# Kernel optimization log

Hardware: AMD Instinct MI355X
Metric: run time of the kernel (lower is better)

## Reference

```python
import jax, jax.numpy as jnp
import numpy as np

N_NODES = 100000
N_EDGES = 800000
IN_CH, HID_CH, OUT_CH = 128, 256, 128


def setup_inputs() -> dict:
    key = jax.random.key(0)
    ks = jax.random.split(key, 8)
    x = jax.random.normal(ks[0], (N_NODES, IN_CH), dtype=jnp.float32)
    edge_index = jax.random.randint(ks[1], (2, N_EDGES), 0, N_NODES, dtype=jnp.int64)
    def lin(k, fan_in, fan_out):
        bound = 1.0 / np.sqrt(fan_in)
        return jax.random.uniform(k, (fan_out, fan_in), minval=-bound, maxval=bound, dtype=jnp.float32)
    # PyG SAGEConv: lin_l (neighbor branch, with bias), lin_r (root branch, no bias)
    W1l = lin(ks[2], IN_CH, HID_CH)
    b1l = jnp.zeros((HID_CH,), dtype=jnp.float32)
    W1r = lin(ks[3], IN_CH, HID_CH)
    W2l = lin(ks[4], HID_CH, OUT_CH)
    b2l = jnp.zeros((OUT_CH,), dtype=jnp.float32)
    W2r = lin(ks[5], HID_CH, OUT_CH)
    return {"x": x, "edge_index": edge_index, "W1l": W1l, "b1l": b1l, "W1r": W1r,
            "W2l": W2l, "b2l": b2l, "W2r": W2r}


def _sage_conv(x, src, dst, Wl, bl, Wr):
    # mean-aggregate messages x[src] at dst, then lin_l(agg) + lin_r(x)
    msgs = x[src]                                        # [E, C]
    summed = jax.ops.segment_sum(msgs, dst, num_segments=N_NODES)
    cnt = jax.ops.segment_sum(jnp.ones((src.shape[0],), dtype=x.dtype), dst, num_segments=N_NODES)
    mean = summed / jnp.maximum(cnt, 1.0)[:, None]       # [N, C]
    return mean @ Wl.T + bl + x @ Wr.T


def reference(x, edge_index, W1l, b1l, W1r, W2l, b2l, W2r):
    src, dst = edge_index[0], edge_index[1]
    h = _sage_conv(x, src, dst, W1l, b1l, W1r)
    h = jax.nn.relu(h)
    # dropout is identity in eval mode (F.dropout with training=False)
    out = _sage_conv(h, src, dst, W2l, b2l, W2r)
    return out
```

## Files before the change

kernel.cpp:

```cpp
#include <hip/hip_runtime.h>

#define N_NODES 100000
#define N_EDGES 800000
#define SCAN_CHUNK 1024
#define SCAN_NB ((N_NODES + SCAN_CHUNK - 1) / SCAN_CHUNK)
#define ROWS_PER_BLK 391
#define TILES 25

typedef __attribute__((ext_vector_type(8))) _Float16 f16x8;
typedef __attribute__((ext_vector_type(4))) _Float16 f16x4;
typedef __attribute__((ext_vector_type(4))) float f32x4;

__global__ void count_int_k(const int* __restrict__ dst, int* __restrict__ cnt, int E) {
    int i = blockIdx.x * blockDim.x + threadIdx.x;
    if (i < E) atomicAdd(&cnt[dst[i]], 1);
}

__global__ __launch_bounds__(256) void scan1_k(const int* __restrict__ cnt,
                                               int* __restrict__ offs,
                                               int* __restrict__ bsums, int N) {
    __shared__ int s[256];
    int t = threadIdx.x;
    int base = blockIdx.x * SCAN_CHUNK + t * 4;
    int v0 = (base + 0 < N) ? cnt[base + 0] : 0;
    int v1 = (base + 1 < N) ? cnt[base + 1] : 0;
    int v2 = (base + 2 < N) ? cnt[base + 2] : 0;
    int v3 = (base + 3 < N) ? cnt[base + 3] : 0;
    int tsum = v0 + v1 + v2 + v3;
    s[t] = tsum;
    __syncthreads();
    for (int off = 1; off < 256; off <<= 1) {
        int val = (t >= off) ? s[t - off] : 0;
        __syncthreads();
        s[t] += val;
        __syncthreads();
    }
    int excl = s[t] - tsum;
    if (base + 0 < N) offs[base + 0] = excl;
    if (base + 1 < N) offs[base + 1] = excl + v0;
    if (base + 2 < N) offs[base + 2] = excl + v0 + v1;
    if (base + 3 < N) offs[base + 3] = excl + v0 + v1 + v2;
    if (t == 255) bsums[blockIdx.x] = s[255];
}

__global__ __launch_bounds__(256) void scan2_k(const int* __restrict__ bsums,
                                               int* __restrict__ boffs, int nb) {
    __shared__ int s[256];
    int t = threadIdx.x;
    int v = (t < nb) ? bsums[t] : 0;
    s[t] = v;
    __syncthreads();
    for (int off = 1; off < 256; off <<= 1) {
        int val = (t >= off) ? s[t - off] : 0;
        __syncthreads();
        s[t] += val;
        __syncthreads();
    }
    if (t < nb) boffs[t] = s[t] - v;
}

__global__ void scan3_k(int* __restrict__ offs, int* __restrict__ cursor,
                        const int* __restrict__ boffs, int N, int E) {
    int i = blockIdx.x * blockDim.x + threadIdx.x;
    if (i < N) {
        int v = offs[i] + boffs[i >> 10];
        offs[i] = v;
        cursor[i] = v;
    }
    if (i == 0) offs[N] = E;
}

__global__ void fill_k(const int* __restrict__ src, const int* __restrict__ dst,
                       int* __restrict__ cursor, int* __restrict__ perm, int E) {
    int e = blockIdx.x * blockDim.x + threadIdx.x;
    if (e < E) {
        int d = dst[e];
        int slot = atomicAdd(&cursor[d], 1);
        perm[slot] = src[e];
    }
}

__global__ __launch_bounds__(256) void cvt_f16_k(const float* __restrict__ in,
                                                 _Float16* __restrict__ outp, int n8) {
    int i = blockIdx.x * blockDim.x + threadIdx.x;
    if (i >= n8) return;
    const float4* p = (const float4*)in + (long long)i * 2;
    float4 v0 = p[0], v1 = p[1];
    f16x8 h;
    h[0] = (_Float16)v0.x; h[1] = (_Float16)v0.y;
    h[2] = (_Float16)v0.z; h[3] = (_Float16)v0.w;
    h[4] = (_Float16)v1.x; h[5] = (_Float16)v1.y;
    h[6] = (_Float16)v1.z; h[7] = (_Float16)v1.w;
    *(f16x8*)&outp[(long long)i * 8] = h;
}

__global__ __launch_bounds__(256) void aggmean_k(const _Float16* __restrict__ feat16,
                                                 const int* __restrict__ perm,
                                                 const int* __restrict__ offs,
                                                 _Float16* __restrict__ m16, int N) {
    int tid = threadIdx.x;
    int node = blockIdx.x * 16 + (tid >> 4);
    int q = tid & 15;
    if (node >= N) return;
    int beg = offs[node], end = offs[node + 1];
    float a[8], b[8];
#pragma unroll
    for (int k = 0; k < 8; k++) { a[k] = 0.0f; b[k] = 0.0f; }
    int i = beg;
    for (; i + 1 < end; i += 2) {
        f16x8 v0 = *(const f16x8*)&feat16[(long long)perm[i] * 128 + q * 8];
        f16x8 v1 = *(const f16x8*)&feat16[(long long)perm[i + 1] * 128 + q * 8];
#pragma unroll
        for (int k = 0; k < 8; k++) { a[k] += (float)v0[k]; b[k] += (float)v1[k]; }
    }
    if (i < end) {
        f16x8 v0 = *(const f16x8*)&feat16[(long long)perm[i] * 128 + q * 8];
#pragma unroll
        for (int k = 0; k < 8; k++) a[k] += (float)v0[k];
    }
    float rc = 1.0f / fmaxf((float)(end - beg), 1.0f);
    f16x8 v;
#pragma unroll
    for (int k = 0; k < 8; k++) v[k] = (_Float16)((a[k] + b[k]) * rc);
    *(f16x8*)&m16[(long long)node * 128 + q * 8] = v;
}

__global__ __launch_bounds__(256) void aggout_k(const _Float16* __restrict__ g16,
                                                const int* __restrict__ perm,
                                                const int* __restrict__ offs,
                                                const _Float16* __restrict__ r2h,
                                                const float* __restrict__ b2l,
                                                float* __restrict__ out, int N) {
    int tid = threadIdx.x;
    int node = blockIdx.x * 16 + (tid >> 4);
    int q = tid & 15;
    if (node >= N) return;
    int beg = offs[node], end = offs[node + 1];
    float a[8], b[8];
#pragma unroll
    for (int k = 0; k < 8; k++) { a[k] = 0.0f; b[k] = 0.0f; }
    int i = beg;
    for (; i + 1 < end; i += 2) {
        f16x8 v0 = *(const f16x8*)&g16[(long long)perm[i] * 128 + q * 8];
        f16x8 v1 = *(const f16x8*)&g16[(long long)perm[i + 1] * 128 + q * 8];
#pragma unroll
        for (int k = 0; k < 8; k++) { a[k] += (float)v0[k]; b[k] += (float)v1[k]; }
    }
    if (i < end) {
        f16x8 v0 = *(const f16x8*)&g16[(long long)perm[i] * 128 + q * 8];
#pragma unroll
        for (int k = 0; k < 8; k++) a[k] += (float)v0[k];
    }
    float rc = 1.0f / fmaxf((float)(end - beg), 1.0f);
    f16x8 rv = *(const f16x8*)&r2h[(long long)node * 128 + q * 8];
    float4 bv0 = ((const float4*)b2l)[q * 2];
    float4 bv1 = ((const float4*)b2l)[q * 2 + 1];
    float4 o0, o1;
    o0.x = (a[0] + b[0]) * rc + (float)rv[0] + bv0.x;
    o0.y = (a[1] + b[1]) * rc + (float)rv[1] + bv0.y;
    o0.z = (a[2] + b[2]) * rc + (float)rv[2] + bv0.z;
    o0.w = (a[3] + b[3]) * rc + (float)rv[3] + bv0.w;
    o1.x = (a[4] + b[4]) * rc + (float)rv[4] + bv1.x;
    o1.y = (a[5] + b[5]) * rc + (float)rv[5] + bv1.y;
    o1.z = (a[6] + b[6]) * rc + (float)rv[6] + bv1.z;
    o1.w = (a[7] + b[7]) * rc + (float)rv[7] + bv1.w;
    ((float4*)out)[(long long)node * 32 + q * 2]     = o0;
    ((float4*)out)[(long long)node * 32 + q * 2 + 1] = o1;
}

__device__ inline void gload16(const void* g, void* l) {
    __builtin_amdgcn_global_load_lds(
        (const __attribute__((address_space(1))) unsigned int*)g,
        (__attribute__((address_space(3))) unsigned int*)l,
        16, 0, 0);
}

template <int LAYER>
__global__ __launch_bounds__(512, 1) void gemm_stream_k(
        const _Float16* __restrict__ Ap0, const _Float16* __restrict__ Ap1,
        const _Float16* __restrict__ Bp0, const _Float16* __restrict__ Bp1,
        const float* __restrict__ bias,
        _Float16* __restrict__ O1h,
        _Float16* __restrict__ OH, int N) {
    __shared__ _Float16 Bs[256 * 256];
    __shared__ _Float16 As3[3][16 * 256];

    const int mbase = blockIdx.x * ROWS_PER_BLK;
    const int rend = min(mbase + ROWS_PER_BLK, N);
    const int tid = threadIdx.x;
    const int lane = tid & 63;
    const int wid = tid >> 6;
    const int lr = lane & 15, lg = lane >> 4;
    const int r2 = lane >> 5;
    const int scs = lane & 31;

    auto STAGE_A = [&](int tt, int bi) {
        int lrow = wid * 2 + r2;
        int ck = scs ^ (lrow & 15);
        int gn = mbase + tt * 16 + lrow;
        if (gn < N) {
            const _Float16* src;
            if constexpr (LAYER == 1)
                src = (ck < 16) ? (Ap0 + (long long)gn * 128 + ck * 8)
                                : (Ap1 + (long long)gn * 128 + (ck - 16) * 8);
            else
                src = Ap0 + (long long)gn * 256 + ck * 8;
            gload16(src, &As3[bi][wid * 512]);
        }
    };

#pragma unroll
    for (int it = 0; it < 16; ++it) {
        int seg = wid * 16 + it;
        int col = seg * 2 + r2;
        int ck = scs ^ (col & 15);
        const _Float16* src;
        if constexpr (LAYER == 1)
            src = (ck < 16) ? (Bp0 + (long long)col * 128 + ck * 8)
                            : (Bp1 + (long long)col * 128 + (ck - 16) * 8);
        else
            src = (col < 128) ? (Bp0 + (long long)col * 256 + ck * 8)
                              : (Bp1 + (long long)(col - 128) * 256 + ck * 8);
        gload16(src, &Bs[seg * 512]);
    }
    STAGE_A(0, 0);
    STAGE_A(1, 1);
    asm volatile("s_waitcnt vmcnt(1)" ::: "memory");
    __builtin_amdgcn_s_barrier();

#pragma unroll 1
    for (int t = 0; t < TILES; ++t) {
        if (t + 2 < TILES) {
            STAGE_A(t + 2, (t + 2) % 3);
            asm volatile("s_waitcnt vmcnt(2)" ::: "memory");
        } else if (t + 1 < TILES) {
            asm volatile("s_waitcnt vmcnt(1)" ::: "memory");
        } else {
            asm volatile("s_waitcnt vmcnt(0)" ::: "memory");
        }
        __builtin_amdgcn_sched_barrier(0);
        __builtin_amdgcn_s_barrier();

        const _Float16* Ab = &As3[t % 3][0];
        f32x4 acc[2];
        acc[0] = (f32x4)0.0f;
        acc[1] = (f32x4)0.0f;
#pragma unroll
        for (int ks = 0; ks < 8; ++ks) {
            int c = ks * 4 + lg;
            f16x8 af = *(const f16x8*)&Ab[lr * 256 + (c ^ lr) * 8];
#pragma unroll
            for (int fc = 0; fc < 2; ++fc) {
                int col = wid * 32 + fc * 16 + lr;
                f16x8 bf = *(const f16x8*)&Bs[col * 256 + (c ^ (col & 15)) * 8];
                acc[fc] = __builtin_amdgcn_mfma_f32_16x16x32_f16(af, bf, acc[fc], 0, 0, 0);
            }
        }

#pragma unroll
        for (int fc = 0; fc < 2; ++fc) {
            int col = wid * 32 + fc * 16 + lr;
            if constexpr (LAYER == 1) {
                float bv = bias[col];
#pragma unroll
                for (int j = 0; j < 4; ++j) {
                    int row = mbase + t * 16 + lg * 4 + j;
                    if (row < rend)
                        OH[(long long)row * 256 + col] =
                            (_Float16)fmaxf(acc[fc][j] + bv, 0.0f);
                }
            } else {
                _Float16* dp = (col < 128) ? OH : O1h;
                int dcol = col & 127;
#pragma unroll
                for (int j = 0; j < 4; ++j) {
                    int row = mbase + t * 16 + lg * 4 + j;
                    if (row < rend)
                        dp[(long long)row * 128 + dcol] = (_Float16)acc[fc][j];
                }
            }
        }
        __builtin_amdgcn_s_barrier();
    }
}

extern "C" void kernel_launch(void* const* d_in, const int* in_sizes, int n_in,
                              void* d_out, int out_size, void* d_ws, size_t ws_size,
                              hipStream_t stream) {
    const float* x   = (const float*)d_in[0];
    const int*   ei  = (const int*)d_in[1];
    const float* W1l = (const float*)d_in[2];
    const float* b1l = (const float*)d_in[3];
    const float* W1r = (const float*)d_in[4];
    const float* W2l = (const float*)d_in[5];
    const float* b2l = (const float*)d_in[6];
    const float* W2r = (const float*)d_in[7];
    float* out = (float*)d_out;

    const int N = N_NODES, E = N_EDGES;
    const int* srcI = ei;
    const int* dstI = ei + E;

    char* ws = (char*)d_ws;
    size_t off = 0;
    auto alloc = [&](size_t bytes) {
        size_t o = off;
        off += (bytes + 511) & ~(size_t)511;
        return o;
    };
    size_t off_cnt   = alloc((size_t)N * 4);
    size_t off_offs  = alloc((size_t)(N + 1) * 4);
    size_t off_cur   = alloc((size_t)N * 4);
    size_t off_bsum  = alloc((size_t)SCAN_NB * 4);
    size_t off_boff  = alloc((size_t)SCAN_NB * 4);
    size_t off_perm  = alloc((size_t)E * 4);
    size_t off_x16   = alloc((size_t)N * 128 * 2);
    size_t off_m16   = alloc((size_t)N * 128 * 2);
    size_t off_h16   = alloc((size_t)N * 256 * 2);
    size_t off_g16   = alloc((size_t)N * 128 * 2);
    size_t off_r2    = alloc((size_t)N * 128 * 2);
    size_t off_w     = alloc((size_t)4 * 32768 * 2);
    int*      cntI = (int*)(ws + off_cnt);
    int*      offs = (int*)(ws + off_offs);
    int*      cur  = (int*)(ws + off_cur);
    int*      bsum = (int*)(ws + off_bsum);
    int*      boff = (int*)(ws + off_boff);
    int*      perm = (int*)(ws + off_perm);
    _Float16* x16  = (_Float16*)(ws + off_x16);
    _Float16* m16  = (_Float16*)(ws + off_m16);
    _Float16* h16  = (_Float16*)(ws + off_h16);
    _Float16* g16  = (_Float16*)(ws + off_g16);
    _Float16* r2h  = (_Float16*)(ws + off_r2);
    _Float16* wbuf = (_Float16*)(ws + off_w);
    const int WSZ = 32768;
    _Float16* w1l16 = wbuf;            _Float16* w1r16 = wbuf + WSZ;
    _Float16* w2l16 = wbuf + 2 * WSZ;  _Float16* w2r16 = wbuf + 3 * WSZ;

    (void)hipMemsetAsync(cntI, 0, (size_t)N * 4, stream);
    count_int_k<<<(E + 255) / 256, 256, 0, stream>>>(dstI, cntI, E);
    scan1_k<<<SCAN_NB, 256, 0, stream>>>(cntI, offs, bsum, N);
    scan2_k<<<1, 256, 0, stream>>>(bsum, boff, SCAN_NB);
    scan3_k<<<(N + 255) / 256, 256, 0, stream>>>(offs, cur, boff, N, E);
    fill_k<<<(E + 255) / 256, 256, 0, stream>>>(srcI, dstI, cur, perm, E);

    {
        int n8x = N * 16;
        cvt_f16_k<<<(n8x + 255) / 256, 256, 0, stream>>>(x, x16, n8x);
        int n8w = 32768 / 8;
        cvt_f16_k<<<(n8w + 255) / 256, 256, 0, stream>>>(W1l, w1l16, n8w);
        cvt_f16_k<<<(n8w + 255) / 256, 256, 0, stream>>>(W1r, w1r16, n8w);
        cvt_f16_k<<<(n8w + 255) / 256, 256, 0, stream>>>(W2l, w2l16, n8w);
        cvt_f16_k<<<(n8w + 255) / 256, 256, 0, stream>>>(W2r, w2r16, n8w);
    }

    aggmean_k<<<(N + 15) / 16, 256, 0, stream>>>(x16, perm, offs, m16, N);
    gemm_stream_k<1><<<256, 512, 0, stream>>>(m16, x16, w1l16, w1r16,
                                              b1l, nullptr, h16, N);

    gemm_stream_k<2><<<256, 512, 0, stream>>>(h16, h16, w2l16, w2r16,
                                              nullptr, r2h, g16, N);
    aggout_k<<<(N + 15) / 16, 256, 0, stream>>>(g16, perm, offs, r2h, b2l, out, N);
}
```

Baseline: 268.4 us.

## Load A fragments directly to registers and split row tiles across two wave groups

The GEMM kernel drops the triple-buffered LDS staging of A tiles and the per-tile block barriers. Each wave now loads its A fragments straight from global memory into registers. The block grows to 1024 threads: 16 waves split into two groups that take alternating row tiles while sharing the resident B matrix in LDS. This removes barrier synchronisation and LDS traffic for A, so the two wave groups can interleave and hide each other's memory latency. The cost is that each of the 8 column waves reloads the same A rows from global/L2, and the larger block raises register pressure.

```diff
diff --git a/kernel.cpp b/kernel.cpp
--- a/kernel.cpp
+++ b/kernel.cpp
@@ -176,42 +176,28 @@
 }
 
 template <int LAYER>
-__global__ __launch_bounds__(512, 1) void gemm_stream_k(
+__global__ __launch_bounds__(1024, 1) void gemm_stream_k(
         const _Float16* __restrict__ Ap0, const _Float16* __restrict__ Ap1,
         const _Float16* __restrict__ Bp0, const _Float16* __restrict__ Bp1,
         const float* __restrict__ bias,
         _Float16* __restrict__ O1h,
         _Float16* __restrict__ OH, int N) {
     __shared__ _Float16 Bs[256 * 256];
-    __shared__ _Float16 As3[3][16 * 256];
 
     const int mbase = blockIdx.x * ROWS_PER_BLK;
     const int rend = min(mbase + ROWS_PER_BLK, N);
     const int tid = threadIdx.x;
     const int lane = tid & 63;
     const int wid = tid >> 6;
+    const int cw = wid & 7;
+    const int rs = wid >> 3;
     const int lr = lane & 15, lg = lane >> 4;
     const int r2 = lane >> 5;
     const int scs = lane & 31;
 
-    auto STAGE_A = [&](int tt, int bi) {
-        int lrow = wid * 2 + r2;
-        int ck = scs ^ (lrow & 15);
-        int gn = mbase + tt * 16 + lrow;
-        if (gn < N) {
-            const _Float16* src;
-            if constexpr (LAYER == 1)
-                src = (ck < 16) ? (Ap0 + (long long)gn * 128 + ck * 8)
-                                : (Ap1 + (long long)gn * 128 + (ck - 16) * 8);
-            else
-                src = Ap0 + (long long)gn * 256 + ck * 8;
-            gload16(src, &As3[bi][wid * 512]);
-        }
-    };
-
-#pragma unroll
-    for (int it = 0; it < 16; ++it) {
-        int seg = wid * 16 + it;
+#pragma unroll
+    for (int it = 0; it < 8; ++it) {
+        int seg = wid * 8 + it;
         int col = seg * 2 + r2;
         int ck = scs ^ (col & 15);
         const _Float16* src;
@@ -223,43 +209,42 @@
                               : (Bp1 + (long long)(col - 128) * 256 + ck * 8);
         gload16(src, &Bs[seg * 512]);
     }
-    STAGE_A(0, 0);
-    STAGE_A(1, 1);
-    asm volatile("s_waitcnt vmcnt(1)" ::: "memory");
-    __builtin_amdgcn_s_barrier();
+    __syncthreads();
 
 #pragma unroll 1
-    for (int t = 0; t < TILES; ++t) {
-        if (t + 2 < TILES) {
-            STAGE_A(t + 2, (t + 2) % 3);
-            asm volatile("s_waitcnt vmcnt(2)" ::: "memory");
-        } else if (t + 1 < TILES) {
-            asm volatile("s_waitcnt vmcnt(1)" ::: "memory");
-        } else {
-            asm volatile("s_waitcnt vmcnt(0)" ::: "memory");
+    for (int t = rs; t < TILES; t += 2) {
+        int gn = mbase + t * 16 + lr;
+        bool rowok = (gn < N);
+        f16x8 af[8];
+#pragma unroll
+        for (int ks = 0; ks < 8; ++ks) {
+            const _Float16* src;
+            if constexpr (LAYER == 1) {
+                src = (ks < 4) ? (Ap0 + (long long)gn * 128 + ks * 32 + lg * 8)
+                               : (Ap1 + (long long)gn * 128 + (ks - 4) * 32 + lg * 8);
+            } else {
+                src = Ap0 + (long long)gn * 256 + ks * 32 + lg * 8;
+            }
+            af[ks] = rowok ? *(const f16x8*)src : (f16x8)(_Float16)0.0f;
         }
-        __builtin_amdgcn_sched_barrier(0);
-        __builtin_amdgcn_s_barrier();
-
-        const _Float16* Ab = &As3[t % 3][0];
+
         f32x4 acc[2];
         acc[0] = (f32x4)0.0f;
         acc[1] = (f32x4)0.0f;
 #pragma unroll
         for (int ks = 0; ks < 8; ++ks) {
             int c = ks * 4 + lg;
-            f16x8 af = *(const f16x8*)&Ab[lr * 256 + (c ^ lr) * 8];
 #pragma unroll
             for (int fc = 0; fc < 2; ++fc) {
-                int col = wid * 32 + fc * 16 + lr;
+                int col = cw * 32 + fc * 16 + lr;
                 f16x8 bf = *(const f16x8*)&Bs[col * 256 + (c ^ (col & 15)) * 8];
-                acc[fc] = __builtin_amdgcn_mfma_f32_16x16x32_f16(af, bf, acc[fc], 0, 0, 0);
+                acc[fc] = __builtin_amdgcn_mfma_f32_16x16x32_f16(af[ks], bf, acc[fc], 0, 0, 0);
             }
         }
 
 #pragma unroll
         for (int fc = 0; fc < 2; ++fc) {
-            int col = wid * 32 + fc * 16 + lr;
+            int col = cw * 32 + fc * 16 + lr;
             if constexpr (LAYER == 1) {
                 float bv = bias[col];
 #pragma unroll
@@ -280,7 +265,6 @@
                 }
             }
         }
-        __builtin_amdgcn_s_barrier();
     }
 }
 
@@ -354,10 +338,10 @@
     }
 
     aggmean_k<<<(N + 15) / 16, 256, 0, stream>>>(x16, perm, offs, m16, N);
-    gemm_stream_k<1><<<256, 512, 0, stream>>>(m16, x16, w1l16, w1r16,
-                                              b1l, nullptr, h16, N);
-
-    gemm_stream_k<2><<<256, 512, 0, stream>>>(h16, h16, w2l16, w2r16,
-                                              nullptr, r2h, g16, N);
+    gemm_stream_k<1><<<256, 1024, 0, stream>>>(m16, x16, w1l16, w1r16,
+                                               b1l, nullptr, h16, N);
+
+    gemm_stream_k<2><<<256, 1024, 0, stream>>>(h16, h16, w2l16, w2r16,
+                                               nullptr, r2h, g16, N);
     aggout_k<<<(N + 15) / 16, 256, 0, stream>>>(g16, perm, offs, r2h, b2l, out, N);
 }
```

Result: slower. 298.9 us (+11.3%).
